# Optimization experiments

Measured on AMD Instinct MI355X. Metric: run time of the kernel, lower is better.

Reference implementation:

```python
import jax, jax.numpy as jnp
import numpy as np

N = 100000      # nodes
E = 1600000     # edges (avg degree 16)
D = 64          # feature dim


def setup_inputs() -> dict:
    key = jax.random.key(0)
    k1, k2, k3, k4 = jax.random.split(key, 4)
    x = jax.random.normal(k1, (N, D), dtype=jnp.float32)
    indices = jax.random.randint(k2, (E,), 0, N, dtype=jnp.int64)
    # valid CSR indptr: sorted, starts at 0, ends at E
    inner = jnp.sort(jax.random.randint(k3, (N - 1,), 0, E, dtype=jnp.int64))
    indptr = jnp.concatenate([
        jnp.zeros((1,), dtype=jnp.int64),
        inner,
        jnp.full((1,), E, dtype=jnp.int64),
    ])
    values = jax.random.normal(k4, (E,), dtype=jnp.float32)
    return {"x": x, "indptr": indptr, "indices": indices, "values": values}


def reference(x, indptr, indices, values):
    # CSR SpMM: out[i] = sum_{k in [indptr[i], indptr[i+1])} values[k] * x[indices[k]]
    num_edges = indices.shape[0]
    num_nodes = indptr.shape[0] - 1
    # recover row id of each edge from indptr (CSR row decompression)
    row = jnp.searchsorted(indptr, jnp.arange(num_edges, dtype=indptr.dtype), side='right') - 1
    gathered = values[:, None] * x[indices]            # [E, D] irregular gather
    out = jax.ops.segment_sum(gathered, row, num_segments=num_nodes)  # [N, D]
    return out
```

## Files before the change

### kernel.cpp

```cpp
#include <hip/hip_runtime.h>
#include <hip/hip_fp16.h>

#define DIM 64

__global__ __launch_bounds__(256) void cvt_half_kernel(
    const float* __restrict__ x, __half* __restrict__ xh, int n4)
{
    int i = blockIdx.x * blockDim.x + threadIdx.x;
    const int stride = gridDim.x * blockDim.x;
    for (; i < n4; i += stride) {
        const float4 v = ((const float4*)x)[i];
        __half2 h0 = __floats2half2_rn(v.x, v.y);
        __half2 h1 = __floats2half2_rn(v.z, v.w);
        uint2 u;
        u.x = *(const unsigned int*)&h0;
        u.y = *(const unsigned int*)&h1;
        ((uint2*)xh)[i] = u;
    }
}

__global__ __launch_bounds__(256) void spmm_half_kernel(
    const __half* __restrict__ xh,
    const int*   __restrict__ indptr,
    const int*   __restrict__ indices,
    const float* __restrict__ values,
    float*       __restrict__ out,
    int n_nodes)
{
    const int row  = (int)((blockIdx.x * blockDim.x + threadIdx.x) >> 6);
    const int lane = (int)(threadIdx.x & 63);
    if (row >= n_nodes) return;
    const int g = lane >> 3;
    const int t = lane & 7;

    const int start = indptr[row];
    const int end   = indptr[row + 1];

    float a[8] = {0.f,0.f,0.f,0.f,0.f,0.f,0.f,0.f};

    if (start < end) {
        const int last = end - 1;
        for (int k = start; k < end; k += 16) {
            const int e0 = k + g;
            const int e1 = k + 8 + g;
            const int i0 = (e0 <= last) ? e0 : last;
            const int i1 = (e1 <= last) ? e1 : last;
            const int c0 = indices[i0];
            const int c1 = indices[i1];
            const float w0 = (e0 <= last) ? values[i0] : 0.0f;
            const float w1 = (e1 <= last) ? values[i1] : 0.0f;

            const uint4 p0 = *(const uint4*)(xh + (((unsigned)c0) << 6) + (t << 3));
            const uint4 p1 = *(const uint4*)(xh + (((unsigned)c1) << 6) + (t << 3));

            const __half* h0 = (const __half*)&p0;
            const __half* h1 = (const __half*)&p1;
#pragma unroll
            for (int j = 0; j < 8; ++j) a[j] += __half2float(h0[j]) * w0;
#pragma unroll
            for (int j = 0; j < 8; ++j) a[j] += __half2float(h1[j]) * w1;
        }
    }

#define RED(m) a[0]+=__shfl_xor(a[0],m); a[1]+=__shfl_xor(a[1],m); \
               a[2]+=__shfl_xor(a[2],m); a[3]+=__shfl_xor(a[3],m); \
               a[4]+=__shfl_xor(a[4],m); a[5]+=__shfl_xor(a[5],m); \
               a[6]+=__shfl_xor(a[6],m); a[7]+=__shfl_xor(a[7],m);
    RED(8) RED(16) RED(32)
#undef RED

    if (lane < 8) {
        float4 r0; r0.x=a[0]; r0.y=a[1]; r0.z=a[2]; r0.w=a[3];
        float4 r1; r1.x=a[4]; r1.y=a[5]; r1.z=a[6]; r1.w=a[7];
        float* dst = out + (((size_t)row) << 6) + (t << 3);
        *(float4*)(dst)     = r0;
        *(float4*)(dst + 4) = r1;
    }
}

__global__ __launch_bounds__(256) void spmm_quad_kernel(
    const float* __restrict__ x,
    const int*   __restrict__ indptr,
    const int*   __restrict__ indices,
    const float* __restrict__ values,
    float*       __restrict__ out,
    int n_nodes)
{
    const int row  = (int)((blockIdx.x * blockDim.x + threadIdx.x) >> 6);
    const int lane = (int)(threadIdx.x & 63);
    if (row >= n_nodes) return;

    const int start = indptr[row];
    const int end   = indptr[row + 1];
    const int g     = lane >> 4;
    const unsigned col4 = (unsigned)(lane & 15) << 2;

    float ax = 0.f, ay = 0.f, az = 0.f, aw = 0.f;

    if (start < end) {
        const int last = end - 1;
        for (int k = start; k < end; k += 16) {
            const int e0 = k +  0 + g, e1 = k + 4 + g, e2 = k + 8 + g, e3 = k + 12 + g;
            const int ce0 = e0 <= last ? e0 : last;
            const int ce1 = e1 <= last ? e1 : last;
            const int ce2 = e2 <= last ? e2 : last;
            const int ce3 = e3 <= last ? e3 : last;
            const int c0 = indices[ce0], c1 = indices[ce1];
            const int c2 = indices[ce2], c3 = indices[ce3];
            const float w0 = (e0 <= last) ? values[ce0] : 0.0f;
            const float w1 = (e1 <= last) ? values[ce1] : 0.0f;
            const float w2 = (e2 <= last) ? values[ce2] : 0.0f;
            const float w3 = (e3 <= last) ? values[ce3] : 0.0f;
            const float4 a0 = *(const float4*)(x + (((unsigned)c0) << 6) + col4);
            const float4 a1 = *(const float4*)(x + (((unsigned)c1) << 6) + col4);
            const float4 a2 = *(const float4*)(x + (((unsigned)c2) << 6) + col4);
            const float4 a3 = *(const float4*)(x + (((unsigned)c3) << 6) + col4);
            ax += w0 * a0.x; ay += w0 * a0.y; az += w0 * a0.z; aw += w0 * a0.w;
            ax += w1 * a1.x; ay += w1 * a1.y; az += w1 * a1.z; aw += w1 * a1.w;
            ax += w2 * a2.x; ay += w2 * a2.y; az += w2 * a2.z; aw += w2 * a2.w;
            ax += w3 * a3.x; ay += w3 * a3.y; az += w3 * a3.z; aw += w3 * a3.w;
        }
    }

    ax += __shfl_xor(ax, 16); ay += __shfl_xor(ay, 16);
    az += __shfl_xor(az, 16); aw += __shfl_xor(aw, 16);
    ax += __shfl_xor(ax, 32); ay += __shfl_xor(ay, 32);
    az += __shfl_xor(az, 32); aw += __shfl_xor(aw, 32);

    if (lane < 16) {
        float4 r; r.x = ax; r.y = ay; r.z = az; r.w = aw;
        *(float4*)(out + ((size_t)row << 6) + col4) = r;
    }
}

extern "C" void kernel_launch(void* const* d_in, const int* in_sizes, int n_in,
                              void* d_out, int out_size, void* d_ws, size_t ws_size,
                              hipStream_t stream) {
    const float* x       = (const float*)d_in[0];
    const int*   indptr  = (const int*)  d_in[1];
    const int*   indices = (const int*)  d_in[2];
    const float* values  = (const float*)d_in[3];
    float*       out     = (float*)d_out;

    const int n_nodes = in_sizes[1] - 1;
    const int n_xelem = in_sizes[0];

    const int threads = 256;
    const int rows_per_block = threads / 64;
    const int blocks = (n_nodes + rows_per_block - 1) / rows_per_block;

    const size_t needed = (size_t)n_xelem * sizeof(__half);
    if (ws_size >= needed) {
        __half* xh = (__half*)d_ws;
        const int n4 = n_xelem / 4;
        cvt_half_kernel<<<2048, 256, 0, stream>>>(x, xh, n4);
        spmm_half_kernel<<<blocks, threads, 0, stream>>>(
            xh, indptr, indices, values, out, n_nodes);
    } else {
        spmm_quad_kernel<<<blocks, threads, 0, stream>>>(
            x, indptr, indices, values, out, n_nodes);
    }
}
```

Measured before the change: 52.68 us.

## Sort column indices per row and balance rows across waves by edge count

Adds a per-call kernel that bitonic-sorts each row's column indices (and permutes values) with wave shuffles into workspace. A new SpMM kernel splits edges evenly across a fixed number of waves using binary search on indptr, and each wave walks several consecutive rows. The goals are better gather locality and less load imbalance from the skewed row lengths. The cost is an extra kernel that reads and writes all edges, plus serial row loops within each wave.

```diff
diff --git a/kernel.cpp b/kernel.cpp
--- a/kernel.cpp
+++ b/kernel.cpp
@@ -16,6 +16,123 @@
         u.x = *(const unsigned int*)&h0;
         u.y = *(const unsigned int*)&h1;
         ((uint2*)xh)[i] = u;
+    }
+}
+
+__global__ __launch_bounds__(256) void sort_rows_kernel(
+    const int*   __restrict__ indptr,
+    const int*   __restrict__ indices,
+    const float* __restrict__ values,
+    int*         __restrict__ sidx,
+    float*       __restrict__ sval,
+    int n_nodes)
+{
+    const int wave = (int)((blockIdx.x * blockDim.x + threadIdx.x) >> 6);
+    const int lane = (int)(threadIdx.x & 63);
+    if (wave >= n_nodes) return;
+    const int s = indptr[wave];
+    const int e = indptr[wave + 1];
+
+    for (int base = s; base < e; base += 64) {
+        const int m = e - base < 64 ? e - base : 64;
+        int key = 0x7fffffff;
+        float v = 0.f;
+        if (lane < m) {
+            key = (indices[base + lane] << 6) | lane;
+            v   = values[base + lane];
+        }
+#pragma unroll
+        for (int k = 2; k <= 64; k <<= 1) {
+#pragma unroll
+            for (int j = k >> 1; j >= 1; j >>= 1) {
+                const int other = __shfl_xor(key, j);
+                const bool up    = ((lane & k) == 0);
+                const bool lower = ((lane & j) == 0);
+                const int mn = key < other ? key : other;
+                const int mx = key < other ? other : key;
+                key = (up == lower) ? mn : mx;
+            }
+        }
+        const int   src = key & 63;
+        const float sv  = __shfl(v, src);
+        if (lane < m) {
+            sidx[base + lane] = key >> 6;
+            sval[base + lane] = sv;
+        }
+    }
+}
+
+__global__ __launch_bounds__(256, 8) void spmm_half_sorted_kernel(
+    const __half* __restrict__ xh,
+    const int*   __restrict__ indptr,
+    const int*   __restrict__ sidx,
+    const float* __restrict__ sval,
+    float*       __restrict__ out,
+    int n_nodes, int n_edges, int n_waves)
+{
+    const int wave = (int)((blockIdx.x * blockDim.x + threadIdx.x) >> 6);
+    const int lane = (int)(threadIdx.x & 63);
+    if (wave >= n_waves) return;
+    const int g = lane >> 3;
+    const int t = lane & 7;
+
+    const long long T0 = (long long)n_edges * wave / n_waves;
+    const long long T1 = (long long)n_edges * (wave + 1) / n_waves;
+    int lo = 0, hi = n_nodes;
+    while (lo < hi) { int mid = (lo + hi) >> 1; if ((long long)indptr[mid] < T0) lo = mid + 1; else hi = mid; }
+    const int r0 = lo;
+    int r1;
+    if (wave == n_waves - 1) { r1 = n_nodes; }
+    else {
+        lo = r0; hi = n_nodes;
+        while (lo < hi) { int mid = (lo + hi) >> 1; if ((long long)indptr[mid] < T1) lo = mid + 1; else hi = mid; }
+        r1 = lo;
+    }
+
+    for (int row = r0; row < r1; ++row) {
+        const int start = indptr[row];
+        const int end   = indptr[row + 1];
+
+        float a[8] = {0.f,0.f,0.f,0.f,0.f,0.f,0.f,0.f};
+
+        if (start < end) {
+            const int last = end - 1;
+            for (int k = start; k < end; k += 16) {
+                const int e0 = k + g;
+                const int e1 = k + 8 + g;
+                const int i0 = (e0 <= last) ? e0 : last;
+                const int i1 = (e1 <= last) ? e1 : last;
+                const int c0 = sidx[i0];
+                const int c1 = sidx[i1];
+                const float w0 = (e0 <= last) ? sval[i0] : 0.0f;
+                const float w1 = (e1 <= last) ? sval[i1] : 0.0f;
+
+                const uint4 p0 = *(const uint4*)(xh + (((unsigned)c0) << 6) + (t << 3));
+                const uint4 p1 = *(const uint4*)(xh + (((unsigned)c1) << 6) + (t << 3));
+
+                const __half* h0 = (const __half*)&p0;
+                const __half* h1 = (const __half*)&p1;
+#pragma unroll
+                for (int j = 0; j < 8; ++j) a[j] += __half2float(h0[j]) * w0;
+#pragma unroll
+                for (int j = 0; j < 8; ++j) a[j] += __half2float(h1[j]) * w1;
+            }
+        }
+
+#define RED(m) a[0]+=__shfl_xor(a[0],m); a[1]+=__shfl_xor(a[1],m); \
+               a[2]+=__shfl_xor(a[2],m); a[3]+=__shfl_xor(a[3],m); \
+               a[4]+=__shfl_xor(a[4],m); a[5]+=__shfl_xor(a[5],m); \
+               a[6]+=__shfl_xor(a[6],m); a[7]+=__shfl_xor(a[7],m);
+        RED(8) RED(16) RED(32)
+#undef RED
+
+        if (lane < 8) {
+            float4 r0v; r0v.x=a[0]; r0v.y=a[1]; r0v.z=a[2]; r0v.w=a[3];
+            float4 r1v; r1v.x=a[4]; r1v.y=a[5]; r1v.z=a[6]; r1v.w=a[7];
+            float* dst = out + (((size_t)row) << 6) + (t << 3);
+            *(float4*)(dst)     = r0v;
+            *(float4*)(dst + 4) = r1v;
+        }
     }
 }
 
@@ -49,10 +166,8 @@
             const int c1 = indices[i1];
             const float w0 = (e0 <= last) ? values[i0] : 0.0f;
             const float w1 = (e1 <= last) ? values[i1] : 0.0f;
-
             const uint4 p0 = *(const uint4*)(xh + (((unsigned)c0) << 6) + (t << 3));
             const uint4 p1 = *(const uint4*)(xh + (((unsigned)c1) << 6) + (t << 3));
-
             const __half* h0 = (const __half*)&p0;
             const __half* h1 = (const __half*)&p1;
 #pragma unroll
@@ -100,7 +215,7 @@
     if (start < end) {
         const int last = end - 1;
         for (int k = start; k < end; k += 16) {
-            const int e0 = k +  0 + g, e1 = k + 4 + g, e2 = k + 8 + g, e3 = k + 12 + g;
+            const int e0 = k + 0 + g, e1 = k + 4 + g, e2 = k + 8 + g, e3 = k + 12 + g;
             const int ce0 = e0 <= last ? e0 : last;
             const int ce1 = e1 <= last ? e1 : last;
             const int ce2 = e2 <= last ? e2 : last;
@@ -144,20 +259,34 @@
 
     const int n_nodes = in_sizes[1] - 1;
     const int n_xelem = in_sizes[0];
+    const int n_edges = in_sizes[2];
 
     const int threads = 256;
-    const int rows_per_block = threads / 64;
-    const int blocks = (n_nodes + rows_per_block - 1) / rows_per_block;
-
-    const size_t needed = (size_t)n_xelem * sizeof(__half);
-    if (ws_size >= needed) {
+    const int row_blocks = (n_nodes + 3) / 4;
+
+    const size_t xh_bytes   = (size_t)n_xelem * sizeof(__half);
+    const size_t sort_bytes = (size_t)n_edges * (sizeof(int) + sizeof(float));
+
+    if (ws_size >= xh_bytes + sort_bytes) {
+        __half* xh   = (__half*)d_ws;
+        int*    sidx = (int*)((char*)d_ws + xh_bytes);
+        float*  sval = (float*)((char*)sidx + (size_t)n_edges * sizeof(int));
+
+        cvt_half_kernel<<<2048, threads, 0, stream>>>(x, xh, n_xelem / 4);
+        sort_rows_kernel<<<row_blocks, threads, 0, stream>>>(
+            indptr, indices, values, sidx, sval, n_nodes);
+
+        const int blocks  = 2048;
+        const int n_waves = blocks * (threads / 64);
+        spmm_half_sorted_kernel<<<blocks, threads, 0, stream>>>(
+            xh, indptr, sidx, sval, out, n_nodes, n_edges, n_waves);
+    } else if (ws_size >= xh_bytes) {
         __half* xh = (__half*)d_ws;
-        const int n4 = n_xelem / 4;
-        cvt_half_kernel<<<2048, 256, 0, stream>>>(x, xh, n4);
-        spmm_half_kernel<<<blocks, threads, 0, stream>>>(
+        cvt_half_kernel<<<2048, threads, 0, stream>>>(x, xh, n_xelem / 4);
+        spmm_half_kernel<<<row_blocks, threads, 0, stream>>>(
             xh, indptr, indices, values, out, n_nodes);
     } else {
-        spmm_quad_kernel<<<blocks, threads, 0, stream>>>(
+        spmm_quad_kernel<<<row_blocks, threads, 0, stream>>>(
             x, indptr, indices, values, out, n_nodes);
     }
 }
```

New measurement: 93.85 us. +78.1%, slower.

## Use persistent edge-balanced waves with software-pipelined row prefetch in half SpMM

Applied to the files above, without the earlier changes.

Replaces the one-wave-per-row half-precision SpMM with a fixed grid of 8192 waves. Each wave binary-searches indptr to own an equal share of edges, then walks its rows sequentially. Index and value loads are prefetched two rows ahead and the first 16-edge gather one row ahead, so memory latency overlaps with the FMA work of the current row. This trades massive row-level parallelism for fewer in-flight waves, which risks lower memory-level parallelism and longer serial chains per wave.

```diff
diff --git a/kernel.cpp b/kernel.cpp
--- a/kernel.cpp
+++ b/kernel.cpp
@@ -16,6 +16,126 @@
         u.x = *(const unsigned int*)&h0;
         u.y = *(const unsigned int*)&h1;
         ((uint2*)xh)[i] = u;
+    }
+}
+
+#define LOAD_TILE_IDX(S, E, C0, C1, W0, W1)                                    \
+    {                                                                          \
+        const int last_ = (E) - 1;                                             \
+        const int e0_ = (S) + g, e1_ = (S) + 8 + g;                            \
+        int i0_ = e0_ <= last_ ? e0_ : last_; if (i0_ < 0) i0_ = 0;            \
+        int i1_ = e1_ <= last_ ? e1_ : last_; if (i1_ < 0) i1_ = 0;            \
+        C0 = indices[i0_];                                                     \
+        C1 = indices[i1_];                                                     \
+        W0 = (e0_ <= last_) ? values[i0_] : 0.0f;                              \
+        W1 = (e1_ <= last_) ? values[i1_] : 0.0f;                              \
+    }
+
+#define GATHER(C0, C1, P0, P1)                                                 \
+    {                                                                          \
+        P0 = *(const uint4*)(xh + (((unsigned)(C0)) << 6) + (t << 3));         \
+        P1 = *(const uint4*)(xh + (((unsigned)(C1)) << 6) + (t << 3));         \
+    }
+
+#define FMA8(P, W)                                                             \
+    {                                                                          \
+        const __half* h_ = (const __half*)&(P);                                \
+        _Pragma("unroll")                                                      \
+        for (int j = 0; j < 8; ++j) a[j] += __half2float(h_[j]) * (W);         \
+    }
+
+__global__ __launch_bounds__(256) void spmm_half_pipe_kernel(
+    const __half* __restrict__ xh,
+    const int*   __restrict__ indptr,
+    const int*   __restrict__ indices,
+    const float* __restrict__ values,
+    float*       __restrict__ out,
+    int n_nodes, int n_edges, int n_waves)
+{
+    const int wave = (int)((blockIdx.x * blockDim.x + threadIdx.x) >> 6);
+    const int lane = (int)(threadIdx.x & 63);
+    if (wave >= n_waves) return;
+    const int g = lane >> 3;
+    const int t = lane & 7;
+
+    const long long T0 = (long long)n_edges * wave / n_waves;
+    const long long T1 = (long long)n_edges * (wave + 1) / n_waves;
+    int lo = 0, hi = n_nodes;
+    while (lo < hi) { int mid = (lo + hi) >> 1; if ((long long)indptr[mid] < T0) lo = mid + 1; else hi = mid; }
+    const int r0 = lo;
+    int r1;
+    if (wave == n_waves - 1) { r1 = n_nodes; }
+    else {
+        lo = r0; hi = n_nodes;
+        while (lo < hi) { int mid = (lo + hi) >> 1; if ((long long)indptr[mid] < T1) lo = mid + 1; else hi = mid; }
+        r1 = lo;
+    }
+    if (r0 >= r1) return;
+    const int rmax = r1 - 1;
+
+    const int rB = (r0 + 1 <= rmax) ? r0 + 1 : rmax;
+    const int rX = (r0 + 2 <= rmax) ? r0 + 2 : rmax;
+    int sC = indptr[r0];  int eC = indptr[r0 + 1];
+    int sN = indptr[rB];  int eN = indptr[rB + 1];
+    int s2 = indptr[rX];  int e2 = indptr[rX + 1];
+
+    int   cA0, cA1, cB0, cB1;
+    float wA0, wA1, wB0, wB1;
+    LOAD_TILE_IDX(sC, eC, cA0, cA1, wA0, wA1)
+    LOAD_TILE_IDX(sN, eN, cB0, cB1, wB0, wB1)
+    uint4 pA0, pA1;
+    GATHER(cA0, cA1, pA0, pA1)
+
+    for (int rC = r0; rC < r1; ++rC) {
+        int r3 = rC + 3; if (r3 > rmax) r3 = rmax;
+        const int s3 = indptr[r3];
+        const int e3 = indptr[r3 + 1];
+
+        uint4 pB0, pB1;
+        GATHER(cB0, cB1, pB0, pB1)
+
+        int cC0, cC1; float wC0, wC1;
+        LOAD_TILE_IDX(s2, e2, cC0, cC1, wC0, wC1)
+
+        float a[8] = {0.f,0.f,0.f,0.f,0.f,0.f,0.f,0.f};
+        FMA8(pA0, wA0)
+        FMA8(pA1, wA1)
+
+        {
+            const int last_ = eC - 1;
+            for (int k = sC + 16; k < eC; k += 16) {
+                const int e0_ = k + g, e1_ = k + 8 + g;
+                const int i0_ = e0_ <= last_ ? e0_ : last_;
+                const int i1_ = e1_ <= last_ ? e1_ : last_;
+                const int c0_ = indices[i0_];
+                const int c1_ = indices[i1_];
+                const float w0_ = (e0_ <= last_) ? values[i0_] : 0.0f;
+                const float w1_ = (e1_ <= last_) ? values[i1_] : 0.0f;
+                uint4 q0, q1;
+                GATHER(c0_, c1_, q0, q1)
+                FMA8(q0, w0_)
+                FMA8(q1, w1_)
+            }
+        }
+
+#define RED(m) a[0]+=__shfl_xor(a[0],m); a[1]+=__shfl_xor(a[1],m); \
+               a[2]+=__shfl_xor(a[2],m); a[3]+=__shfl_xor(a[3],m); \
+               a[4]+=__shfl_xor(a[4],m); a[5]+=__shfl_xor(a[5],m); \
+               a[6]+=__shfl_xor(a[6],m); a[7]+=__shfl_xor(a[7],m);
+        RED(8) RED(16) RED(32)
+#undef RED
+        if (lane < 8) {
+            float4 v0; v0.x=a[0]; v0.y=a[1]; v0.z=a[2]; v0.w=a[3];
+            float4 v1; v1.x=a[4]; v1.y=a[5]; v1.z=a[6]; v1.w=a[7];
+            float* dst = out + (((size_t)rC) << 6) + (t << 3);
+            *(float4*)(dst)     = v0;
+            *(float4*)(dst + 4) = v1;
+        }
+
+        sC = sN; eC = eN; sN = s2; eN = e2; s2 = s3; e2 = e3;
+        cA0 = cB0; cA1 = cB1; wA0 = wB0; wA1 = wB1;
+        pA0 = pB0; pA1 = pB1;
+        cB0 = cC0; cB1 = cC1; wB0 = wC0; wB1 = wC1;
     }
 }
 
@@ -49,16 +169,10 @@
             const int c1 = indices[i1];
             const float w0 = (e0 <= last) ? values[i0] : 0.0f;
             const float w1 = (e1 <= last) ? values[i1] : 0.0f;
-
             const uint4 p0 = *(const uint4*)(xh + (((unsigned)c0) << 6) + (t << 3));
             const uint4 p1 = *(const uint4*)(xh + (((unsigned)c1) << 6) + (t << 3));
-
-            const __half* h0 = (const __half*)&p0;
-            const __half* h1 = (const __half*)&p1;
-#pragma unroll
-            for (int j = 0; j < 8; ++j) a[j] += __half2float(h0[j]) * w0;
-#pragma unroll
-            for (int j = 0; j < 8; ++j) a[j] += __half2float(h1[j]) * w1;
+            FMA8(p0, w0)
+            FMA8(p1, w1)
         }
     }
 
@@ -100,7 +214,7 @@
     if (start < end) {
         const int last = end - 1;
         for (int k = start; k < end; k += 16) {
-            const int e0 = k +  0 + g, e1 = k + 4 + g, e2 = k + 8 + g, e3 = k + 12 + g;
+            const int e0 = k + 0 + g, e1 = k + 4 + g, e2 = k + 8 + g, e3 = k + 12 + g;
             const int ce0 = e0 <= last ? e0 : last;
             const int ce1 = e1 <= last ? e1 : last;
             const int ce2 = e2 <= last ? e2 : last;
@@ -144,20 +258,22 @@
 
     const int n_nodes = in_sizes[1] - 1;
     const int n_xelem = in_sizes[0];
+    const int n_edges = in_sizes[2];
 
     const int threads = 256;
-    const int rows_per_block = threads / 64;
-    const int blocks = (n_nodes + rows_per_block - 1) / rows_per_block;
-
-    const size_t needed = (size_t)n_xelem * sizeof(__half);
-    if (ws_size >= needed) {
+
+    const size_t xh_bytes = (size_t)n_xelem * sizeof(__half);
+    if (ws_size >= xh_bytes) {
         __half* xh = (__half*)d_ws;
-        const int n4 = n_xelem / 4;
-        cvt_half_kernel<<<2048, 256, 0, stream>>>(x, xh, n4);
-        spmm_half_kernel<<<blocks, threads, 0, stream>>>(
-            xh, indptr, indices, values, out, n_nodes);
+        cvt_half_kernel<<<2048, threads, 0, stream>>>(x, xh, n_xelem / 4);
+
+        const int blocks  = 2048;
+        const int n_waves = blocks * (threads / 64);
+        spmm_half_pipe_kernel<<<blocks, threads, 0, stream>>>(
+            xh, indptr, indices, values, out, n_nodes, n_edges, n_waves);
     } else {
-        spmm_quad_kernel<<<blocks, threads, 0, stream>>>(
+        const int row_blocks = (n_nodes + 3) / 4;
+        spmm_quad_kernel<<<row_blocks, threads, 0, stream>>>(
             x, indptr, indices, values, out, n_nodes);
     }
 }
```

After: 74.97 us. +42.3%, slower.

## Bucket edges by column panel and sweep panels in lockstep for gather locality

Applied to the files above, without the earlier changes.

Adds a bucketing pass that reorders each row's (column, value) pairs by column panel (column >> 14) into a workspace buffer. A new sweep kernel then processes rows panel by panel across all blocks, so that concurrent gathers hit a narrower slice of the fp16 feature matrix and stay in cache. This costs an extra kernel that reads indices and values and writes an 8-byte-per-edge pair array, plus a loop synchronised per panel with wave-wide any-checks, in exchange for better L2/MALL locality on the random gathers.

```diff
diff --git a/kernel.cpp b/kernel.cpp
--- a/kernel.cpp
+++ b/kernel.cpp
@@ -2,6 +2,10 @@
 #include <hip/hip_fp16.h>
 
 #define DIM 64
+#define PSHIFT 14
+#define NPAN 8
+#define NR 4
+#define SWEEP_BLOCKS 1024
 
 __global__ __launch_bounds__(256) void cvt_half_kernel(
     const float* __restrict__ x, __half* __restrict__ xh, int n4)
@@ -16,6 +20,138 @@
         u.x = *(const unsigned int*)&h0;
         u.y = *(const unsigned int*)&h1;
         ((uint2*)xh)[i] = u;
+    }
+}
+
+__global__ __launch_bounds__(256) void bucket_kernel(
+    const int*   __restrict__ indptr,
+    const int*   __restrict__ indices,
+    const float* __restrict__ values,
+    uint2*       __restrict__ spair,
+    int n_nodes)
+{
+    const int wave = (int)((blockIdx.x * blockDim.x + threadIdx.x) >> 6);
+    const int lane = (int)(threadIdx.x & 63);
+    const int sub  = lane >> 4;
+    const int sl   = lane & 15;
+    const int row  = wave * 4 + sub;
+
+    int s = 0, e = 0;
+    if (row < n_nodes) { s = indptr[row]; e = indptr[row + 1]; }
+    const int shift = sub * 16;
+    const unsigned below = (1u << sl) - 1u;
+
+#define SEGB(P) ((unsigned)((__ballot(key == (P)) >> shift) & 0xFFFFull))
+
+    int c0=0,c1=0,c2=0,c3=0,c4=0,c5=0,c6=0,c7=0;
+    for (int base = s; base < e; base += 16) {
+        const int kk = base + sl;
+        const bool val = kk < e;
+        const int key = val ? (indices[kk] >> PSHIFT) : NPAN;
+        c0 += __popc(SEGB(0)); c1 += __popc(SEGB(1));
+        c2 += __popc(SEGB(2)); c3 += __popc(SEGB(3));
+        c4 += __popc(SEGB(4)); c5 += __popc(SEGB(5));
+        c6 += __popc(SEGB(6)); c7 += __popc(SEGB(7));
+    }
+    int u0 = 0;
+    int u1 = c0;
+    int u2 = u1 + c1;
+    int u3 = u2 + c2;
+    int u4 = u3 + c3;
+    int u5 = u4 + c4;
+    int u6 = u5 + c5;
+    int u7 = u6 + c6;
+
+    for (int base = s; base < e; base += 16) {
+        const int kk = base + sl;
+        const bool val = kk < e;
+        const int c = val ? indices[kk] : 0;
+        const float v = val ? values[kk] : 0.0f;
+        const int key = val ? (c >> PSHIFT) : NPAN;
+        const unsigned m0 = SEGB(0), m1 = SEGB(1), m2 = SEGB(2), m3 = SEGB(3);
+        const unsigned m4 = SEGB(4), m5 = SEGB(5), m6 = SEGB(6), m7 = SEGB(7);
+        unsigned mk = m0; int uk = u0;
+        mk = (key==1)?m1:mk; uk = (key==1)?u1:uk;
+        mk = (key==2)?m2:mk; uk = (key==2)?u2:uk;
+        mk = (key==3)?m3:mk; uk = (key==3)?u3:uk;
+        mk = (key==4)?m4:mk; uk = (key==4)?u4:uk;
+        mk = (key==5)?m5:mk; uk = (key==5)?u5:uk;
+        mk = (key==6)?m6:mk; uk = (key==6)?u6:uk;
+        mk = (key==7)?m7:mk; uk = (key==7)?u7:uk;
+        if (val) {
+            uint2 pr; pr.x = (unsigned)c; pr.y = __float_as_uint(v);
+            spair[s + uk + (int)__popc(mk & below)] = pr;
+        }
+        u0 += __popc(m0); u1 += __popc(m1); u2 += __popc(m2); u3 += __popc(m3);
+        u4 += __popc(m4); u5 += __popc(m5); u6 += __popc(m6); u7 += __popc(m7);
+    }
+#undef SEGB
+}
+
+__global__ __launch_bounds__(256, 4) void sweep_kernel(
+    const __half* __restrict__ xh,
+    const int*    __restrict__ indptr,
+    const uint2*  __restrict__ spair,
+    float*        __restrict__ out,
+    int n_nodes, int rows_pb)
+{
+    const int b  = blockIdx.x;
+    const int gq = (int)(threadIdx.x >> 3);
+    const int t  = (int)(threadIdx.x & 7);
+    const int rbase = b * rows_pb;
+
+    int kk[NR], ke[NR];
+    float a[NR][8];
+#pragma unroll
+    for (int i = 0; i < NR; ++i) {
+        const int rl = gq + 32 * i;
+        const int r  = rbase + rl;
+        const bool ok = (rl < rows_pb) && (r < n_nodes);
+        kk[i] = ok ? indptr[r] : 0;
+        ke[i] = ok ? indptr[r + 1] : 0;
+#pragma unroll
+        for (int j = 0; j < 8; ++j) a[i][j] = 0.f;
+    }
+
+    for (int p = 0; p < NPAN; ++p) {
+        while (true) {
+            uint2 pk[NR]; uint4 g[NR]; bool in[NR];
+            bool anyl = false;
+#pragma unroll
+            for (int i = 0; i < NR; ++i) {
+                const int addr = (kk[i] < ke[i]) ? kk[i] : 0;
+                pk[i] = spair[addr];
+            }
+#pragma unroll
+            for (int i = 0; i < NR; ++i) {
+                in[i] = (kk[i] < ke[i]) && ((int)(pk[i].x >> PSHIFT) == p);
+                const unsigned cu = in[i] ? pk[i].x : 0u;
+                g[i] = *(const uint4*)(xh + ((size_t)cu << 6) + (t << 3));
+            }
+#pragma unroll
+            for (int i = 0; i < NR; ++i) {
+                const float vv = in[i] ? __uint_as_float(pk[i].y) : 0.f;
+                const __half* h = (const __half*)&g[i];
+#pragma unroll
+                for (int j = 0; j < 8; ++j) a[i][j] += __half2float(h[j]) * vv;
+                kk[i] += in[i] ? 1 : 0;
+                anyl = anyl || in[i];
+            }
+            if (!__any(anyl)) break;
+        }
+    }
+
+#pragma unroll
+    for (int i = 0; i < NR; ++i) {
+        const int rl = gq + 32 * i;
+        const int r  = rbase + rl;
+        if ((rl < rows_pb) && (r < n_nodes)) {
+            float4 r0; r0.x = a[i][0]; r0.y = a[i][1]; r0.z = a[i][2]; r0.w = a[i][3];
+            float4 r1; r1.x = a[i][4]; r1.y = a[i][5]; r1.z = a[i][6]; r1.w = a[i][7];
+            float* dst = out + (((size_t)r) << 6) + (t << 3);
+            *(float4*)(dst)     = r0;
+            *(float4*)(dst + 4) = r1;
+        }
     }
 }
 
@@ -49,10 +185,8 @@
             const int c1 = indices[i1];
             const float w0 = (e0 <= last) ? values[i0] : 0.0f;
             const float w1 = (e1 <= last) ? values[i1] : 0.0f;
-
             const uint4 p0 = *(const uint4*)(xh + (((unsigned)c0) << 6) + (t << 3));
             const uint4 p1 = *(const uint4*)(xh + (((unsigned)c1) << 6) + (t << 3));
-
             const __half* h0 = (const __half*)&p0;
             const __half* h1 = (const __half*)&p1;
 #pragma unroll
@@ -100,7 +234,7 @@
     if (start < end) {
         const int last = end - 1;
         for (int k = start; k < end; k += 16) {
-            const int e0 = k +  0 + g, e1 = k + 4 + g, e2 = k + 8 + g, e3 = k + 12 + g;
+            const int e0 = k + 0 + g, e1 = k + 4 + g, e2 = k + 8 + g, e3 = k + 12 + g;
             const int ce0 = e0 <= last ? e0 : last;
             const int ce1 = e1 <= last ? e1 : last;
             const int ce2 = e2 <= last ? e2 : last;
@@ -144,20 +278,40 @@
 
     const int n_nodes = in_sizes[1] - 1;
     const int n_xelem = in_sizes[0];
+    const int n_edges = in_sizes[2];
 
     const int threads = 256;
-    const int rows_per_block = threads / 64;
-    const int blocks = (n_nodes + rows_per_block - 1) / rows_per_block;
-
-    const size_t needed = (size_t)n_xelem * sizeof(__half);
-    if (ws_size >= needed) {
+    const int rows_pb = (n_nodes + SWEEP_BLOCKS - 1) / SWEEP_BLOCKS;
+
+    const size_t xh_bytes    = (size_t)n_xelem * sizeof(__half);
+    const size_t spair_bytes = (size_t)n_edges * sizeof(uint2);
+
+    const bool sweep_ok = (ws_size >= xh_bytes + spair_bytes) &&
+                          (n_nodes <= (1 << (PSHIFT + 3))) &&
+                          (rows_pb <= 32 * NR);
+
+    if (sweep_ok) {
+        __half* xh    = (__half*)d_ws;
+        uint2*  spair = (uint2*)((char*)d_ws + xh_bytes);
+
+        cvt_half_kernel<<<2048, threads, 0, stream>>>(x, xh, n_xelem / 4);
+
+        const int bwaves  = (n_nodes + 3) / 4;
+        const int bblocks = (bwaves + 3) / 4;
+        bucket_kernel<<<bblocks, threads, 0, stream>>>(
+            indptr, indices, values, spair, n_nodes);
+
+        sweep_kernel<<<SWEEP_BLOCKS, threads, 0, stream>>>(
+            xh, indptr, spair, out, n_nodes, rows_pb);
+    } else if (ws_size >= xh_bytes) {
         __half* xh = (__half*)d_ws;
-        const int n4 = n_xelem / 4;
-        cvt_half_kernel<<<2048, 256, 0, stream>>>(x, xh, n4);
-        spmm_half_kernel<<<blocks, threads, 0, stream>>>(
+        cvt_half_kernel<<<2048, threads, 0, stream>>>(x, xh, n_xelem / 4);
+        const int row_blocks = (n_nodes + 3) / 4;
+        spmm_half_kernel<<<row_blocks, threads, 0, stream>>>(
             xh, indptr, indices, values, out, n_nodes);
     } else {
-        spmm_quad_kernel<<<blocks, threads, 0, stream>>>(
+        const int row_blocks = (n_nodes + 3) / 4;
+        spmm_quad_kernel<<<row_blocks, threads, 0, stream>>>(
             x, indptr, indices, values, out, n_nodes);
     }
 }
```

After: 194.5 us. +269.3%, slower.
